# Kernel tuning notes

Hardware: AMD Instinct MI355X
Metric: run time of the kernel (lower is better)

The kernel has to match this reference:

```python
import jax, jax.numpy as jnp
import numpy as np

N, S, K, H, D = 8192, 16384, 16, 8, 512
E = N * K
HEAD_DIM = D // H


def setup_inputs() -> dict:
    key = jax.random.key(0)
    ks = jax.random.split(key, 12)
    x = jax.random.normal(ks[0], (N, D), jnp.float32)
    # every destination row gets K edges so softmax rows are never empty
    row_index = jnp.repeat(jnp.arange(N, dtype=jnp.int32), K)  # [E], sorted
    src_index = jax.random.randint(ks[1], (E,), 0, S, dtype=jnp.int32)
    att_bias = jax.random.normal(ks[2], (H, E), jnp.float32)
    dist = jax.random.uniform(ks[3], (E,), jnp.float32, minval=0.5, maxval=10.0)
    pos = jax.random.normal(ks[4], (N, 3), jnp.float32)
    src_pos = jax.random.normal(ks[5], (S, 3), jnp.float32)
    org_to_src = jax.random.randint(ks[6], (S,), 0, N, dtype=jnp.int32)
    scale = 1.0 / np.sqrt(D).astype(np.float32)
    Wq = jax.random.normal(ks[7], (D, D), jnp.float32) * scale
    bq = jax.random.normal(ks[8], (D,), jnp.float32) * 0.01
    Wk = jax.random.normal(ks[9], (D, D), jnp.float32) * scale
    bk = jax.random.normal(ks[10], (D,), jnp.float32) * 0.01
    return {"x": x, "row_index": row_index, "src_index": src_index,
            "att_bias": att_bias, "dist": dist, "pos": pos, "src_pos": src_pos,
            "org_to_src": org_to_src, "Wq": Wq, "bq": bq, "Wk": Wk, "bk": bk}


def reference(x, row_index, src_index, att_bias, dist, pos, src_pos, org_to_src,
              Wq, bq, Wk, bk):
    n, d_model = x.shape
    h, e = att_bias.shape
    hd = d_model // h
    # Projections -> [N, H, hd]; key gathered to the source list via org_to_src -> [S, H, hd]
    q = (x @ Wq + bq).reshape(n, h, hd)
    k_src = ((x @ Wk + bk).reshape(n, h, hd))[org_to_src]
    # Per-edge masked logits: (q/sqrt(hd)) . k + att_bias   (COO sparse attention)
    q_e = q[row_index]                       # [E, H, hd]
    k_e = k_src[src_index]                   # [E, H, hd]
    logits = jnp.einsum('ehd,ehd->eh', q_e, k_e) / np.sqrt(hd).astype(np.float32)
    logits = logits + att_bias.T             # [E, H]
    # Segment softmax over edges sharing a destination row
    m = jax.ops.segment_max(logits, row_index, num_segments=n)      # [N, H]
    p = jnp.exp(logits - m[row_index])
    z = jax.ops.segment_sum(p, row_index, num_segments=n)           # [N, H]
    att = p / z[row_index]                                          # [E, H]
    # Distance reweighting: 1/dist with dist==0 -> 0 weight
    safe = jnp.where(dist == 0, 1.0, dist)
    inv_d = jnp.where(dist == 0, 0.0, 1.0 / safe)
    att = att * inv_d[:, None]
    # dst_vec = att @ src_pos ; src_vec = (att @ 1) * pos   (both as segment sums)
    dst = jax.ops.segment_sum(att[:, :, None] * src_pos[src_index][:, None, :],
                              row_index, num_segments=n)            # [N, H, 3]
    asum = jax.ops.segment_sum(att, row_index, num_segments=n)      # [N, H]
    feat = dst - asum[:, :, None] * pos[:, None, :]                 # [N, H, 3]
    return feat.reshape(n, h * 3)
```

## Files before the change

### kernel.cpp

```cpp
#include <hip/hip_runtime.h>

#define N_ROWS 8192
#define D_MODEL 512
#define KT 512
#define NHEAD 8
#define KEDGE 16
#define NEDGE (N_ROWS * KEDGE)
#define BK 64

using f32x4  = __attribute__((ext_vector_type(4))) float;
using bf16x8 = __attribute__((ext_vector_type(8))) __bf16;
using u16x8  = __attribute__((ext_vector_type(8))) unsigned short;

__device__ __forceinline__ unsigned short bf16_rtne(float f) {
    unsigned u = __float_as_uint(f);
    u += 0x7FFFu + ((u >> 16) & 1u);
    return (unsigned short)(u >> 16);
}
__device__ __forceinline__ float from_bf16(unsigned short b) {
    return __uint_as_float(((unsigned)b) << 16);
}

#define GLOAD16(gp, lp) __builtin_amdgcn_global_load_lds( \
    (__attribute__((address_space(1))) void*)(void*)(gp), \
    (__attribute__((address_space(3))) void*)(lp), 16, 0, 0)

__global__ __launch_bounds__(256) void prep(const float* __restrict__ x,
                                            const float* __restrict__ Wq,
                                            const float* __restrict__ Wk,
                                            unsigned short* __restrict__ Xb,
                                            unsigned short* __restrict__ Bt) {
    if (blockIdx.x < 2048) {
        const int i = (blockIdx.x * 256 + threadIdx.x) * 8;
        const float4 a = *reinterpret_cast<const float4*>(x + i);
        const float4 b = *reinterpret_cast<const float4*>(x + i + 4);
        u16x8 o;
        o[0] = bf16_rtne(a.x); o[1] = bf16_rtne(a.y);
        o[2] = bf16_rtne(a.z); o[3] = bf16_rtne(a.w);
        o[4] = bf16_rtne(b.x); o[5] = bf16_rtne(b.y);
        o[6] = bf16_rtne(b.z); o[7] = bf16_rtne(b.w);
        *reinterpret_cast<u16x8*>(Xb + i) = o;
    } else {
        const int gid = (blockIdx.x - 2048) * 256 + threadIdx.x;
        const int j = gid >> 9;
        const int k = gid & 511;
        const float* W = (j < 512) ? Wq : Wk;
        Bt[(size_t)j * KT + k] = bf16_rtne(W[k * D_MODEL + (j & 511)]);
    }
}

__global__ __launch_bounds__(512) void gemm_qk(
    const unsigned short* __restrict__ Xb, const unsigned short* __restrict__ Bt,
    const float* __restrict__ bq, const float* __restrict__ bk,
    unsigned short* __restrict__ Qp, unsigned short* __restrict__ Kp)
{
    __shared__ __align__(16) unsigned short As[2][128 * BK];
    __shared__ __align__(16) unsigned short Bs[2][128 * BK];

    const int tid  = threadIdx.x;
    const int lane = tid & 63;
    const int wave = tid >> 6;
    const int wr   = wave >> 2;
    const int wc   = wave & 3;

    const int bid = blockIdx.x;
    const int xcd = bid & 7;
    const int j   = bid >> 3;
    const int rp  = xcd * 8 + (j >> 3);
    const int cp  = j & 7;
    const int row0 = rp * 128, col0 = cp * 128;

    f32x4 acc[4][2];
    #pragma unroll
    for (int m = 0; m < 4; ++m)
        #pragma unroll
        for (int n = 0; n < 2; ++n)
            acc[m][n] = (f32x4){0.f, 0.f, 0.f, 0.f};

    const int crow = tid >> 3;
    const int sc   = ((tid & 7) ^ (crow & 7)) * 8;

    const unsigned short* gA = Xb + (size_t)(row0 + crow) * D_MODEL + sc;
    const unsigned short* gB = Bt + (size_t)(col0 + crow) * KT     + sc;

    #define STAGE(b, kb) do { \
        GLOAD16(gA + (kb),                &As[b][tid * 8]); \
        GLOAD16(gA + (kb) + 64 * D_MODEL, &As[b][(tid + 512) * 8]); \
        GLOAD16(gB + (kb),                &Bs[b][tid * 8]); \
        GLOAD16(gB + (kb) + 64 * KT,      &Bs[b][(tid + 512) * 8]); \
    } while (0)

    STAGE(0, 0);
    __syncthreads();

    int buf = 0;
    for (int kt = 0; kt < KT / BK; ++kt) {
        if (kt < KT / BK - 1) STAGE(buf ^ 1, (kt + 1) * BK);
        #pragma unroll
        for (int kk = 0; kk < 2; ++kk) {
            const int kc = kk * 4 + (lane >> 4);
            bf16x8 afr[4], bfr[2];
            #pragma unroll
            for (int m = 0; m < 4; ++m) {
                const int r = wr * 64 + m * 16 + (lane & 15);
                afr[m] = __builtin_bit_cast(bf16x8, *reinterpret_cast<const u16x8*>(
                    &As[buf][r * BK + ((kc ^ (r & 7)) * 8)]));
            }
            #pragma unroll
            for (int n = 0; n < 2; ++n) {
                const int r = wc * 32 + n * 16 + (lane & 15);
                bfr[n] = __builtin_bit_cast(bf16x8, *reinterpret_cast<const u16x8*>(
                    &Bs[buf][r * BK + ((kc ^ (r & 7)) * 8)]));
            }
            #pragma unroll
            for (int m = 0; m < 4; ++m)
                #pragma unroll
                for (int n = 0; n < 2; ++n)
                    acc[m][n] = __builtin_amdgcn_mfma_f32_16x16x32_bf16(
                        afr[m], bfr[n], acc[m][n], 0, 0, 0);
        }
        __syncthreads();
        buf ^= 1;
    }
    #undef STAGE

    #pragma unroll
    for (int m = 0; m < 4; ++m) {
        const int row = row0 + wr * 64 + m * 16 + (lane >> 4) * 4;
        #pragma unroll
        for (int n = 0; n < 2; ++n) {
            const int c = col0 + wc * 32 + n * 16 + (lane & 15);
            const int cc = c & 511;
            unsigned short* plane = (c < 512) ? Qp : Kp;
            const float bias = (c < 512) ? bq[cc] : bk[cc];
            #pragma unroll
            for (int r = 0; r < 4; ++r)
                plane[(size_t)(row + r) * D_MODEL + cc] = bf16_rtne(acc[m][n][r] + bias);
        }
    }
}

__global__ __launch_bounds__(256) void edge_kernel(
    const unsigned short* __restrict__ Qp, const unsigned short* __restrict__ Kp,
    const int* __restrict__ src_index,
    const int* __restrict__ org_to_src,
    const float* __restrict__ att_bias,
    const float* __restrict__ dist,
    const float* __restrict__ pos,
    const float* __restrict__ src_pos,
    float* __restrict__ out)
{
    const int lane = threadIdx.x & 63;
    const int wave = threadIdx.x >> 6;
    const int n = blockIdx.x * 4 + wave;
    const int ll = lane & 31;
    const int half = lane >> 5;
    const int h = ll >> 2;
    const int o1 = h * 64 + (ll & 3) * 8;
    const int o2 = o1 + 32;

    int se[8], kne[8];
    #pragma unroll
    for (int i = 0; i < 8; ++i) se[i] = src_index[n * KEDGE + 2 * i + half];
    const u16x8 q1 = *reinterpret_cast<const u16x8*>(Qp + (size_t)n * D_MODEL + o1);
    const u16x8 q2 = *reinterpret_cast<const u16x8*>(Qp + (size_t)n * D_MODEL + o2);
    #pragma unroll
    for (int i = 0; i < 8; ++i) kne[i] = org_to_src[se[i]];

    u16x8 kv1[8], kv2[8];
    #pragma unroll
    for (int i = 0; i < 8; ++i) {
        const unsigned short* kp = Kp + (size_t)kne[i] * D_MODEL;
        kv1[i] = *reinterpret_cast<const u16x8*>(kp + o1);
        kv2[i] = *reinterpret_cast<const u16x8*>(kp + o2);
    }

    float qf1[8], qf2[8];
    #pragma unroll
    for (int i = 0; i < 8; ++i) { qf1[i] = from_bf16(q1[i]); qf2[i] = from_bf16(q2[i]); }

    float logit[8];
    #pragma unroll
    for (int i = 0; i < 8; ++i) {
        float p = 0.f;
        #pragma unroll
        for (int jj = 0; jj < 8; ++jj)
            p += qf1[jj] * from_bf16(kv1[i][jj]) + qf2[jj] * from_bf16(kv2[i][jj]);
        p += __shfl_xor(p, 1);
        p += __shfl_xor(p, 2);
        logit[i] = p * 0.125f;
    }

    float iv[8], spx[8], spy[8], spz[8];
    #pragma unroll
    for (int i = 0; i < 8; ++i) {
        const int ge = n * KEDGE + 2 * i + half;
        logit[i] += att_bias[(size_t)h * NEDGE + ge];
        const float d = dist[ge];
        iv[i] = (d == 0.f) ? 0.f : 1.f / d;
        const int s = se[i];
        spx[i] = src_pos[s * 3 + 0];
        spy[i] = src_pos[s * 3 + 1];
        spz[i] = src_pos[s * 3 + 2];
    }

    float mx = logit[0];
    #pragma unroll
    for (int i = 1; i < 8; ++i) mx = fmaxf(mx, logit[i]);
    mx = fmaxf(mx, __shfl_xor(mx, 32));
    float pe[8];
    float z = 0.f;
    #pragma unroll
    for (int i = 0; i < 8; ++i) { pe[i] = __expf(logit[i] - mx); z += pe[i]; }
    z += __shfl_xor(z, 32);
    const float rz = 1.f / z;

    float d0 = 0.f, d1 = 0.f, d2 = 0.f, asum = 0.f;
    #pragma unroll
    for (int i = 0; i < 8; ++i) {
        const float w = pe[i] * rz * iv[i];
        d0 += w * spx[i]; d1 += w * spy[i]; d2 += w * spz[i];
        asum += w;
    }
    d0 += __shfl_xor(d0, 32);
    d1 += __shfl_xor(d1, 32);
    d2 += __shfl_xor(d2, 32);
    asum += __shfl_xor(asum, 32);

    const int c = ll & 3;
    if (half == 0 && c < 3) {
        const float dc = (c == 0) ? d0 : ((c == 1) ? d1 : d2);
        out[n * 24 + h * 3 + c] = dc - asum * pos[n * 3 + c];
    }
}

extern "C" void kernel_launch(void* const* d_in, const int* in_sizes, int n_in,
                              void* d_out, int out_size, void* d_ws, size_t ws_size,
                              hipStream_t stream) {
    const float* x          = (const float*)d_in[0];
    const int*   src_index  = (const int*)d_in[2];
    const float* att_bias   = (const float*)d_in[3];
    const float* dist       = (const float*)d_in[4];
    const float* pos        = (const float*)d_in[5];
    const float* src_pos    = (const float*)d_in[6];
    const int*   org_to_src = (const int*)d_in[7];
    const float* Wq         = (const float*)d_in[8];
    const float* bq         = (const float*)d_in[9];
    const float* Wk         = (const float*)d_in[10];
    const float* bk         = (const float*)d_in[11];
    float* out = (float*)d_out;

    char* ws = (char*)d_ws;
    unsigned short* Xb  = (unsigned short*)(ws);
    unsigned short* Bt  = (unsigned short*)(ws + ( 8u << 20));
    unsigned short* Qp  = (unsigned short*)(ws + ( 9u << 20));
    unsigned short* Kp  = (unsigned short*)(ws + (17u << 20));

    prep<<<dim3(4096), dim3(256), 0, stream>>>(x, Wq, Wk, Xb, Bt);
    gemm_qk<<<dim3(512), dim3(512), 0, stream>>>(Xb, Bt, bq, bk, Qp, Kp);
    edge_kernel<<<dim3(N_ROWS / 4), dim3(256), 0, stream>>>(
        Qp, Kp, src_index, org_to_src, att_bias, dist, pos, src_pos, out);
}
```

Baseline: 41.22 us.

## Split each row's edges across two waves with LDS softmax reduction

The edge kernel now assigns each destination row to two waves, each handling 8 of the 16 edges. Per-head max, sum and the position partials are combined through shared memory, with three block barriers added. The aim is to double the number of waves and cut per-thread gather chains, so the latency of the dependent src_index -> org_to_src -> Kp gathers is hidden better. In exchange it adds barrier and LDS overhead and launches twice as many blocks.

```diff
diff --git a/kernel.cpp b/kernel.cpp
--- a/kernel.cpp
+++ b/kernel.cpp
@@ -150,26 +150,33 @@
     const float* __restrict__ src_pos,
     float* __restrict__ out)
 {
+    __shared__ float smax[2][2][NHEAD];
+    __shared__ float ssum[2][2][NHEAD];
+    __shared__ float spart[2][2][NHEAD][4];
+
     const int lane = threadIdx.x & 63;
     const int wave = threadIdx.x >> 6;
-    const int n = blockIdx.x * 4 + wave;
-    const int ll = lane & 31;
+    const int rl   = wave >> 1;
+    const int sub  = wave & 1;
+    const int n    = blockIdx.x * 2 + rl;
+    const int ll   = lane & 31;
     const int half = lane >> 5;
-    const int h = ll >> 2;
-    const int o1 = h * 64 + (ll & 3) * 8;
-    const int o2 = o1 + 32;
-
-    int se[8], kne[8];
-    #pragma unroll
-    for (int i = 0; i < 8; ++i) se[i] = src_index[n * KEDGE + 2 * i + half];
+    const int h    = ll >> 2;
+    const int o1   = h * 64 + (ll & 3) * 8;
+    const int o2   = o1 + 32;
+
+    int se[4], kne[4];
+    #pragma unroll
+    for (int i = 0; i < 4; ++i)
+        se[i] = src_index[n * KEDGE + sub * 8 + 2 * i + half];
     const u16x8 q1 = *reinterpret_cast<const u16x8*>(Qp + (size_t)n * D_MODEL + o1);
     const u16x8 q2 = *reinterpret_cast<const u16x8*>(Qp + (size_t)n * D_MODEL + o2);
     #pragma unroll
-    for (int i = 0; i < 8; ++i) kne[i] = org_to_src[se[i]];
-
-    u16x8 kv1[8], kv2[8];
-    #pragma unroll
-    for (int i = 0; i < 8; ++i) {
+    for (int i = 0; i < 4; ++i) kne[i] = org_to_src[se[i]];
+
+    u16x8 kv1[4], kv2[4];
+    #pragma unroll
+    for (int i = 0; i < 4; ++i) {
         const unsigned short* kp = Kp + (size_t)kne[i] * D_MODEL;
         kv1[i] = *reinterpret_cast<const u16x8*>(kp + o1);
         kv2[i] = *reinterpret_cast<const u16x8*>(kp + o2);
@@ -179,23 +186,23 @@
     #pragma unroll
     for (int i = 0; i < 8; ++i) { qf1[i] = from_bf16(q1[i]); qf2[i] = from_bf16(q2[i]); }
 
-    float logit[8];
-    #pragma unroll
-    for (int i = 0; i < 8; ++i) {
+    float logit[4];
+    #pragma unroll
+    for (int i = 0; i < 4; ++i) {
         float p = 0.f;
         #pragma unroll
         for (int jj = 0; jj < 8; ++jj)
             p += qf1[jj] * from_bf16(kv1[i][jj]) + qf2[jj] * from_bf16(kv2[i][jj]);
         p += __shfl_xor(p, 1);
         p += __shfl_xor(p, 2);
-        logit[i] = p * 0.125f;
-    }
-
-    float iv[8], spx[8], spy[8], spz[8];
-    #pragma unroll
-    for (int i = 0; i < 8; ++i) {
-        const int ge = n * KEDGE + 2 * i + half;
-        logit[i] += att_bias[(size_t)h * NEDGE + ge];
+        logit[i] = p * 0.125f
+                 + att_bias[(size_t)h * NEDGE + n * KEDGE + sub * 8 + 2 * i + half];
+    }
+
+    float iv[4], spx[4], spy[4], spz[4];
+    #pragma unroll
+    for (int i = 0; i < 4; ++i) {
+        const int ge = n * KEDGE + sub * 8 + 2 * i + half;
         const float d = dist[ge];
         iv[i] = (d == 0.f) ? 0.f : 1.f / d;
         const int s = se[i];
@@ -206,18 +213,25 @@
 
     float mx = logit[0];
     #pragma unroll
-    for (int i = 1; i < 8; ++i) mx = fmaxf(mx, logit[i]);
+    for (int i = 1; i < 4; ++i) mx = fmaxf(mx, logit[i]);
     mx = fmaxf(mx, __shfl_xor(mx, 32));
-    float pe[8];
+    if (half == 0 && (ll & 3) == 0) smax[rl][sub][h] = mx;
+    __syncthreads();
+    mx = fmaxf(mx, smax[rl][sub ^ 1][h]);
+
+    float pe[4];
     float z = 0.f;
     #pragma unroll
-    for (int i = 0; i < 8; ++i) { pe[i] = __expf(logit[i] - mx); z += pe[i]; }
+    for (int i = 0; i < 4; ++i) { pe[i] = __expf(logit[i] - mx); z += pe[i]; }
     z += __shfl_xor(z, 32);
+    if (half == 0 && (ll & 3) == 0) ssum[rl][sub][h] = z;
+    __syncthreads();
+    z += ssum[rl][sub ^ 1][h];
     const float rz = 1.f / z;
 
     float d0 = 0.f, d1 = 0.f, d2 = 0.f, asum = 0.f;
     #pragma unroll
-    for (int i = 0; i < 8; ++i) {
+    for (int i = 0; i < 4; ++i) {
         const float w = pe[i] * rz * iv[i];
         d0 += w * spx[i]; d1 += w * spy[i]; d2 += w * spz[i];
         asum += w;
@@ -228,9 +242,13 @@
     asum += __shfl_xor(asum, 32);
 
     const int c = ll & 3;
-    if (half == 0 && c < 3) {
-        const float dc = (c == 0) ? d0 : ((c == 1) ? d1 : d2);
-        out[n * 24 + h * 3 + c] = dc - asum * pos[n * 3 + c];
+    if (half == 0)
+        spart[rl][sub][h][c] = (c == 0) ? d0 : ((c == 1) ? d1 : ((c == 2) ? d2 : asum));
+    __syncthreads();
+    if (sub == 0 && half == 0 && c < 3) {
+        const float dc = ((c == 0) ? d0 : ((c == 1) ? d1 : d2)) + spart[rl][1][h][c];
+        const float at = asum + spart[rl][1][h][3];
+        out[n * 24 + h * 3 + c] = dc - at * pos[n * 3 + c];
     }
 }
 
@@ -258,6 +276,6 @@
 
     prep<<<dim3(4096), dim3(256), 0, stream>>>(x, Wq, Wk, Xb, Bt);
     gemm_qk<<<dim3(512), dim3(512), 0, stream>>>(Xb, Bt, bq, bk, Qp, Kp);
-    edge_kernel<<<dim3(N_ROWS / 4), dim3(256), 0, stream>>>(
+    edge_kernel<<<dim3(N_ROWS / 2), dim3(256), 0, stream>>>(
         Qp, Kp, src_index, org_to_src, att_bias, dist, pos, src_pos, out);
 }
```

Result: slower. 44.35 us (+7.6%).

## Fuse x bf16 conversion into GEMM A-load and tile-transpose weight prep

Applied to the files above, without the earlier changes.

Drops the separate x-to-bf16 conversion pass. The GEMM now reads fp32 x directly into registers, converts to bf16, and writes swizzled LDS after the MFMA loop, so the global loads overlap with compute. Weight transpose and conversion move to a small LDS-tiled transpose kernel that replaces the uncoalesced strided reads. This removes an 8 MB write and re-read of Xb, at the cost of more register pressure and VALU conversion work inside the GEMM, and the A loads no longer use the direct global-to-LDS path.

```diff
diff --git a/kernel.cpp b/kernel.cpp
--- a/kernel.cpp
+++ b/kernel.cpp
@@ -1,4 +1,5 @@
 #include <hip/hip_runtime.h>
+#include <hip/hip_bf16.h>
 
 #define N_ROWS 8192
 #define D_MODEL 512
@@ -20,37 +21,43 @@
 __device__ __forceinline__ float from_bf16(unsigned short b) {
     return __uint_as_float(((unsigned)b) << 16);
 }
+__device__ __forceinline__ u16x8 cvt8(const float4 a, const float4 b) {
+    u16x8 o;
+    o[0] = __builtin_bit_cast(unsigned short, __float2bfloat16(a.x));
+    o[1] = __builtin_bit_cast(unsigned short, __float2bfloat16(a.y));
+    o[2] = __builtin_bit_cast(unsigned short, __float2bfloat16(a.z));
+    o[3] = __builtin_bit_cast(unsigned short, __float2bfloat16(a.w));
+    o[4] = __builtin_bit_cast(unsigned short, __float2bfloat16(b.x));
+    o[5] = __builtin_bit_cast(unsigned short, __float2bfloat16(b.y));
+    o[6] = __builtin_bit_cast(unsigned short, __float2bfloat16(b.z));
+    o[7] = __builtin_bit_cast(unsigned short, __float2bfloat16(b.w));
+    return o;
+}
 
 #define GLOAD16(gp, lp) __builtin_amdgcn_global_load_lds( \
     (__attribute__((address_space(1))) void*)(void*)(gp), \
     (__attribute__((address_space(3))) void*)(lp), 16, 0, 0)
 
-__global__ __launch_bounds__(256) void prep(const float* __restrict__ x,
-                                            const float* __restrict__ Wq,
-                                            const float* __restrict__ Wk,
-                                            unsigned short* __restrict__ Xb,
-                                            unsigned short* __restrict__ Bt) {
-    if (blockIdx.x < 2048) {
-        const int i = (blockIdx.x * 256 + threadIdx.x) * 8;
-        const float4 a = *reinterpret_cast<const float4*>(x + i);
-        const float4 b = *reinterpret_cast<const float4*>(x + i + 4);
-        u16x8 o;
-        o[0] = bf16_rtne(a.x); o[1] = bf16_rtne(a.y);
-        o[2] = bf16_rtne(a.z); o[3] = bf16_rtne(a.w);
-        o[4] = bf16_rtne(b.x); o[5] = bf16_rtne(b.y);
-        o[6] = bf16_rtne(b.z); o[7] = bf16_rtne(b.w);
-        *reinterpret_cast<u16x8*>(Xb + i) = o;
-    } else {
-        const int gid = (blockIdx.x - 2048) * 256 + threadIdx.x;
-        const int j = gid >> 9;
-        const int k = gid & 511;
-        const float* W = (j < 512) ? Wq : Wk;
-        Bt[(size_t)j * KT + k] = bf16_rtne(W[k * D_MODEL + (j & 511)]);
-    }
+__global__ __launch_bounds__(256) void wprep(const float* __restrict__ Wq,
+                                             const float* __restrict__ Wk,
+                                             unsigned short* __restrict__ Bt) {
+    __shared__ float tile[32][33];
+    const int k0 = blockIdx.x * 32;
+    const int j0 = blockIdx.y * 32;
+    const float* W = (j0 < 512) ? Wq : Wk;
+    const int jj = j0 & 511;
+    const int tx = threadIdx.x & 31, ty = threadIdx.x >> 5;
+    #pragma unroll
+    for (int i = 0; i < 4; ++i)
+        tile[ty + 8 * i][tx] = W[(size_t)(k0 + ty + 8 * i) * D_MODEL + jj + tx];
+    __syncthreads();
+    #pragma unroll
+    for (int i = 0; i < 4; ++i)
+        Bt[(size_t)(j0 + ty + 8 * i) * KT + k0 + tx] = bf16_rtne(tile[tx][ty + 8 * i]);
 }
 
 __global__ __launch_bounds__(512) void gemm_qk(
-    const unsigned short* __restrict__ Xb, const unsigned short* __restrict__ Bt,
+    const float* __restrict__ x, const unsigned short* __restrict__ Bt,
     const float* __restrict__ bq, const float* __restrict__ bk,
     unsigned short* __restrict__ Qp, unsigned short* __restrict__ Kp)
 {
@@ -78,39 +85,54 @@
             acc[m][n] = (f32x4){0.f, 0.f, 0.f, 0.f};
 
     const int crow = tid >> 3;
-    const int sc   = ((tid & 7) ^ (crow & 7)) * 8;
-
-    const unsigned short* gA = Xb + (size_t)(row0 + crow) * D_MODEL + sc;
-    const unsigned short* gB = Bt + (size_t)(col0 + crow) * KT     + sc;
-
-    #define STAGE(b, kb) do { \
-        GLOAD16(gA + (kb),                &As[b][tid * 8]); \
-        GLOAD16(gA + (kb) + 64 * D_MODEL, &As[b][(tid + 512) * 8]); \
-        GLOAD16(gB + (kb),                &Bs[b][tid * 8]); \
-        GLOAD16(gB + (kb) + 64 * KT,      &Bs[b][(tid + 512) * 8]); \
+    const int kc   = tid & 7;
+    const int swz  = (kc ^ (crow & 7)) * 8;
+
+    const float* gx = x + (size_t)(row0 + crow) * D_MODEL + kc * 8;
+    const unsigned short* gB = Bt + (size_t)(col0 + crow) * KT + swz;
+
+    float4 a0, a1, a2, a3;
+
+    #define LOADA(kb) do { \
+        const float* xp = gx + (kb); \
+        a0 = *reinterpret_cast<const float4*>(xp); \
+        a1 = *reinterpret_cast<const float4*>(xp + 4); \
+        a2 = *reinterpret_cast<const float4*>(xp + 64 * D_MODEL); \
+        a3 = *reinterpret_cast<const float4*>(xp + 64 * D_MODEL + 4); \
     } while (0)
-
-    STAGE(0, 0);
+    #define WRITEA(b) do { \
+        *reinterpret_cast<u16x8*>(&As[b][crow * BK + swz])        = cvt8(a0, a1); \
+        *reinterpret_cast<u16x8*>(&As[b][(crow + 64) * BK + swz]) = cvt8(a2, a3); \
+    } while (0)
+    #define STAGEB(b, kb) do { \
+        GLOAD16(gB + (kb),           &Bs[b][tid * 8]); \
+        GLOAD16(gB + (kb) + 64 * KT, &Bs[b][(tid + 512) * 8]); \
+    } while (0)
+
+    LOADA(0);
+    STAGEB(0, 0);
+    WRITEA(0);
     __syncthreads();
 
     int buf = 0;
     for (int kt = 0; kt < KT / BK; ++kt) {
-        if (kt < KT / BK - 1) STAGE(buf ^ 1, (kt + 1) * BK);
+        const bool more = (kt + 1 < KT / BK);
+        if (more) { LOADA((kt + 1) * BK); STAGEB(buf ^ 1, (kt + 1) * BK); }
         #pragma unroll
         for (int kk = 0; kk < 2; ++kk) {
-            const int kc = kk * 4 + (lane >> 4);
+            const int kcl = kk * 4 + (lane >> 4);
             bf16x8 afr[4], bfr[2];
             #pragma unroll
             for (int m = 0; m < 4; ++m) {
                 const int r = wr * 64 + m * 16 + (lane & 15);
                 afr[m] = __builtin_bit_cast(bf16x8, *reinterpret_cast<const u16x8*>(
-                    &As[buf][r * BK + ((kc ^ (r & 7)) * 8)]));
+                    &As[buf][r * BK + ((kcl ^ (r & 7)) * 8)]));
             }
             #pragma unroll
             for (int n = 0; n < 2; ++n) {
                 const int r = wc * 32 + n * 16 + (lane & 15);
                 bfr[n] = __builtin_bit_cast(bf16x8, *reinterpret_cast<const u16x8*>(
-                    &Bs[buf][r * BK + ((kc ^ (r & 7)) * 8)]));
+                    &Bs[buf][r * BK + ((kcl ^ (r & 7)) * 8)]));
             }
             #pragma unroll
             for (int m = 0; m < 4; ++m)
@@ -119,10 +141,13 @@
                     acc[m][n] = __builtin_amdgcn_mfma_f32_16x16x32_bf16(
                         afr[m], bfr[n], acc[m][n], 0, 0, 0);
         }
+        if (more) WRITEA(buf ^ 1);
         __syncthreads();
         buf ^= 1;
     }
-    #undef STAGE
+    #undef LOADA
+    #undef WRITEA
+    #undef STAGEB
 
     #pragma unroll
     for (int m = 0; m < 4; ++m) {
@@ -251,13 +276,12 @@
     float* out = (float*)d_out;
 
     char* ws = (char*)d_ws;
-    unsigned short* Xb  = (unsigned short*)(ws);
-    unsigned short* Bt  = (unsigned short*)(ws + ( 8u << 20));
-    unsigned short* Qp  = (unsigned short*)(ws + ( 9u << 20));
-    unsigned short* Kp  = (unsigned short*)(ws + (17u << 20));
-
-    prep<<<dim3(4096), dim3(256), 0, stream>>>(x, Wq, Wk, Xb, Bt);
-    gemm_qk<<<dim3(512), dim3(512), 0, stream>>>(Xb, Bt, bq, bk, Qp, Kp);
+    unsigned short* Bt  = (unsigned short*)(ws);
+    unsigned short* Qp  = (unsigned short*)(ws + ( 1u << 20));
+    unsigned short* Kp  = (unsigned short*)(ws + ( 9u << 20));
+
+    wprep<<<dim3(16, 32), dim3(256), 0, stream>>>(Wq, Wk, Bt);
+    gemm_qk<<<dim3(512), dim3(512), 0, stream>>>(x, Bt, bq, bk, Qp, Kp);
     edge_kernel<<<dim3(N_ROWS / 4), dim3(256), 0, stream>>>(
         Qp, Kp, src_index, org_to_src, att_bias, dist, pos, src_pos, out);
 }
```

Result: slower. 42.29 us (+2.6%).
